# Optimization experiments

Measured on AMD Instinct MI355X. Metric: run time of the kernel, lower is better.

## Reference

```python
import jax, jax.numpy as jnp
import numpy as np
import math

N, K, M = 4, 2048, 1024   # batch, seq_len, dim_in
DQ, DV = 1024, 1024       # dim_q, dim_v


def _xavier_uniform(k, shape, fan_in, fan_out):
    bound = math.sqrt(6.0 / (fan_in + fan_out))
    return jax.random.uniform(k, shape, jnp.float32, -bound, bound)


def setup_inputs() -> dict:
    key = jax.random.key(0)
    ks = jax.random.split(key, 9)
    query = jax.random.normal(ks[0], (N, K, M), jnp.float32)
    key_t = jax.random.normal(ks[1], (N, K, M), jnp.float32)
    value = jax.random.normal(ks[2], (N, K, M), jnp.float32)
    # causal mask: True above diagonal -> masked out (typical production usage)
    mask = jnp.broadcast_to(jnp.triu(jnp.ones((K, K), bool), k=1), (N, K, K))
    Wq = _xavier_uniform(ks[3], (DQ, M), M, DQ)
    bq = jax.random.uniform(ks[4], (DQ,), jnp.float32, -1 / math.sqrt(M), 1 / math.sqrt(M))
    Wk = _xavier_uniform(ks[5], (DQ, M), M, DQ)
    bk = jax.random.uniform(ks[6], (DQ,), jnp.float32, -1 / math.sqrt(M), 1 / math.sqrt(M))
    Wv = _xavier_uniform(ks[7], (DV, M), M, DV)
    bv = jax.random.uniform(ks[8], (DV,), jnp.float32, -1 / math.sqrt(M), 1 / math.sqrt(M))
    return {"query": query, "key": key_t, "value": value, "mask": mask,
            "Wq": Wq, "bq": bq, "Wk": Wk, "bk": bk, "Wv": Wv, "bv": bv}


def reference(query, key, value, mask, Wq, bq, Wk, bk, Wv, bv):
    # linear projections (torch Linear: x @ W.T + b)
    Q = jnp.einsum("nkm,dm->nkd", query, Wq) + bq   # (N, K, DQ)
    Kp = jnp.einsum("nkm,dm->nkd", key, Wk) + bk    # (N, K, DQ)
    V = jnp.einsum("nkm,dm->nkd", value, Wv) + bv   # (N, K, DV)
    # scaled dot product; scale uses projected dim (dim_q)
    scores = jnp.einsum("nqd,nkd->nqk", Q, Kp) / jnp.sqrt(jnp.float32(DQ))
    scores = jnp.where(mask, jnp.float32(-1e9), scores)
    w = jax.nn.softmax(scores, axis=2)               # (N, K, K)
    y = jnp.einsum("nqk,nkd->nqd", w, V)             # (N, K, DV)
    return y
```

## Files before the change

### kernel.cpp

```cpp
#include <hip/hip_runtime.h>
#include <hip/hip_bf16.h>


typedef __bf16 bf16x8 __attribute__((ext_vector_type(8)));
typedef float  f32x4  __attribute__((ext_vector_type(4)));

#define BM 128
#define BN 128
#define BKK 64

__device__ __forceinline__ int swz(int row, int slot) {
    return row * 128 + (((slot) ^ (row & 7)) << 4);
}

__device__ __forceinline__ void gload16(const __bf16* g, __bf16* l) {
    __builtin_amdgcn_global_load_lds((const __attribute__((address_space(1))) void*)g,
                                     (__attribute__((address_space(3))) void*)l, 16, 0, 0);
}

__device__ __forceinline__ void xcd_remap(int& bx, int& by, int& bz) {
    const int nx = gridDim.x, ny = gridDim.y;
    const int nwg = nx * ny * gridDim.z;
    const int flat = blockIdx.x + nx * (blockIdx.y + ny * blockIdx.z);
    const int q = nwg >> 3, r = nwg & 7;
    const int xcd = flat & 7, idx = flat >> 3;
    const int l = (xcd < r ? xcd * (q + 1) : r * (q + 1) + (xcd - r) * q) + idx;
    bx = l % nx; by = (l / nx) % ny; bz = l / (nx * ny);
}

template<int MH, int NH, bool DOA, bool DOB>
__device__ __forceinline__ void phase256(const char* LAb, const char* LBb,
    int wM, int wn, int g, int li,
    bf16x8 (&aF)[4][2], bf16x8 (&bF)[2][2], f32x4 (&acc)[8][4])
{
    if (DOA) {
#pragma unroll
        for (int i = 0; i < 4; i++)
#pragma unroll
            for (int kk = 0; kk < 2; kk++) {
                const int row = wM * 128 + MH * 64 + i * 16 + li;
                aF[i][kk] = *(const bf16x8*)(LAb + swz(row, kk * 4 + g));
            }
    }
    if (DOB) {
#pragma unroll
        for (int j = 0; j < 2; j++)
#pragma unroll
            for (int kk = 0; kk < 2; kk++) {
                const int row = wn * 64 + NH * 32 + j * 16 + li;
                bF[j][kk] = *(const bf16x8*)(LBb + swz(row, kk * 4 + g));
            }
    }
    __builtin_amdgcn_s_barrier();
    __builtin_amdgcn_sched_barrier(0);
    __builtin_amdgcn_s_setprio(1);
#pragma unroll
    for (int kk = 0; kk < 2; kk++)
#pragma unroll
        for (int i = 0; i < 4; i++)
#pragma unroll
            for (int j = 0; j < 2; j++)
                acc[MH * 4 + i][NH * 2 + j] = __builtin_amdgcn_mfma_f32_16x16x32_bf16(
                    aF[i][kk], bF[j][kk], acc[MH * 4 + i][NH * 2 + j], 0, 0, 0);
    __builtin_amdgcn_s_setprio(0);
    __builtin_amdgcn_s_barrier();
    __builtin_amdgcn_sched_barrier(0);
}

__global__ __launch_bounds__(512)
void gemm256_proj(const __bf16* __restrict__ Ap, const __bf16* __restrict__ Bp,
                  const float* __restrict__ b0, const float* __restrict__ b1,
                  const float* __restrict__ b2, float scaleQ, __bf16* __restrict__ Cp)
{
    __shared__ __bf16 LA[2][256 * 64];
    __shared__ __bf16 LB[2][256 * 64];

    int bx, by, bz;
    xcd_remap(bx, by, bz);
    const int m0 = by * 256, n0 = bx * 256;
    const long z = bz;

    const int tid = threadIdx.x;
    const int wid = tid >> 6, lane = tid & 63;
    const int wM = wid >> 2;
    const int wn = wid & 3;
    const int g = lane >> 4, li = lane & 15;
    const int rl = lane >> 3;
    const int sg = (lane & 7) ^ rl;

    const __bf16* Az = Ap + z * 8388608L;
    const __bf16* Bz = Bp + z * 1048576L;

    auto ISSUE = [&](int buf, int k0) {
#pragma unroll
        for (int i = 0; i < 4; i++) {
            const int seg = wid * 4 + i;
            const int r = seg * 8 + rl;
            gload16(Az + (long)(m0 + r) * 1024 + k0 + sg * 8, &LA[buf][seg * 512]);
        }
#pragma unroll
        for (int i = 0; i < 4; i++) {
            const int seg = wid * 4 + i;
            const int r = seg * 8 + rl;
            gload16(Bz + (long)(n0 + r) * 1024 + k0 + sg * 8, &LB[buf][seg * 512]);
        }
    };

    f32x4 acc[8][4];
#pragma unroll
    for (int i = 0; i < 8; i++)
#pragma unroll
        for (int j = 0; j < 4; j++)
            acc[i][j] = (f32x4){0.f, 0.f, 0.f, 0.f};
    bf16x8 aF[4][2], bF[2][2];

    const int nt = 16;
    ISSUE(0, 0);
    int cur = 0;
    for (int t = 0; t < nt; ++t) {
        if (t + 1 < nt) {
            ISSUE(cur ^ 1, (t + 1) * 64);
            __builtin_amdgcn_sched_barrier(0);
            asm volatile("s_waitcnt vmcnt(8)" ::: "memory");
        } else {
            __builtin_amdgcn_sched_barrier(0);
            asm volatile("s_waitcnt vmcnt(0)" ::: "memory");
        }
        __builtin_amdgcn_sched_barrier(0);
        __builtin_amdgcn_s_barrier();
        __builtin_amdgcn_sched_barrier(0);

        const char* LAb = (const char*)&LA[cur][0];
        const char* LBb = (const char*)&LB[cur][0];
        phase256<0, 0, true,  true >(LAb, LBb, wM, wn, g, li, aF, bF, acc);
        phase256<0, 1, false, true >(LAb, LBb, wM, wn, g, li, aF, bF, acc);
        phase256<1, 1, true,  false>(LAb, LBb, wM, wn, g, li, aF, bF, acc);
        phase256<1, 0, false, true >(LAb, LBb, wM, wn, g, li, aF, bF, acc);
        cur ^= 1;
    }

    const float scale = (z == 0) ? scaleQ : 1.f;
    const float* bias = z == 0 ? b0 : (z == 1 ? b1 : b2);
    __bf16* C = Cp + z * 8388608L;
#pragma unroll
    for (int fi = 0; fi < 8; fi++) {
#pragma unroll
        for (int fj = 0; fj < 4; fj++) {
            const int row = m0 + wM * 128 + fi * 16 + g * 4;
            const int col = n0 + wn * 64 + fj * 16 + li;
            const float b = bias[col];
#pragma unroll
            for (int jj = 0; jj < 4; jj++)
                C[(long)(row + jj) * 1024 + col] = (__bf16)((acc[fi][fj][jj] + b) * scale);
        }
    }
}

template<int MODE>
__global__ __launch_bounds__(256)
void gemm_bt(const __bf16* __restrict__ Ap, const __bf16* __restrict__ Bp,
             void* __restrict__ Cp, int Kd, int lda, int ldb, int ldc,
             long strideA, long strideB, long strideC)
{
    __shared__ __bf16 smA[2][BM * BKK];
    __shared__ __bf16 smB[2][BN * BKK];

    int bx, by, bz;
    xcd_remap(bx, by, bz);

    const int tid = threadIdx.x;
    const int m0 = by * BM;
    const int n0 = bx * BN;
    if (MODE == 1 && n0 > m0) return;

    const long z = bz;
    int kEnd = Kd;
    if (MODE == 2) { int lim = m0 + BM; kEnd = lim < Kd ? lim : Kd; }

    const int wid = tid >> 6, lane = tid & 63;
    const int wm = (wid >> 1) * 64, wn = (wid & 1) * 64;
    const int g = lane >> 4, li = lane & 15;
    const int rl = lane >> 3;
    const int sg = (lane & 7) ^ rl;
    const __bf16* Az = Ap + z * strideA;
    const __bf16* Bz = Bp + z * strideB;

    f32x4 acc[4][4];
    for (int i = 0; i < 4; i++)
        for (int j = 0; j < 4; j++)
            acc[i][j] = (f32x4){0.f, 0.f, 0.f, 0.f};

    auto STAGE = [&](int buf, int k0) {
        for (int i = 0; i < 4; i++) {
            const int seg = i * 4 + wid;
            const int r = seg * 8 + rl;
            gload16(Az + (long)(m0 + r) * lda + k0 + sg * 8, &smA[buf][seg * 512]);
            gload16(Bz + (long)(n0 + r) * ldb + k0 + sg * 8, &smB[buf][seg * 512]);
        }
    };

    auto COMPUTE = [&](int buf) {
        for (int kk = 0; kk < 2; kk++) {
            const int slot = kk * 4 + g;
            bf16x8 af[4], bfv[4];
            for (int t = 0; t < 4; t++)
                af[t] = *(const bf16x8*)((const char*)&smA[buf][0] + swz(wm + t * 16 + li, slot));
            for (int t = 0; t < 4; t++)
                bfv[t] = *(const bf16x8*)((const char*)&smB[buf][0] + swz(wn + t * 16 + li, slot));
            for (int tm = 0; tm < 4; tm++)
                for (int tn = 0; tn < 4; tn++)
                    acc[tm][tn] = __builtin_amdgcn_mfma_f32_16x16x32_bf16(
                        af[tm], bfv[tn], acc[tm][tn], 0, 0, 0);
        }
    };

    const int nt = kEnd / BKK;
    STAGE(0, 0);
    __syncthreads();
    int cur = 0;
    for (int t = 0; t < nt - 1; ++t) {
        STAGE(cur ^ 1, (t + 1) * BKK);
        COMPUTE(cur);
        __syncthreads();
        cur ^= 1;
    }
    COMPUTE(cur);

    for (int tm = 0; tm < 4; tm++) {
        for (int tn = 0; tn < 4; tn++) {
            const int row = m0 + wm + tm * 16 + g * 4;
            const int col = n0 + wn + tn * 16 + li;
            float* C = (float*)Cp + z * strideC;
            for (int j = 0; j < 4; j++)
                C[(long)(row + j) * ldc + col] = acc[tm][tn][j];
        }
    }
}

__global__ __launch_bounds__(256)
void cvt3(const float* __restrict__ s0, const float* __restrict__ s1,
          const float* __restrict__ s2, __bf16* __restrict__ d0,
          __bf16* __restrict__ d1, __bf16* __restrict__ d2, long n)
{
    const int zz = blockIdx.y;
    const float* src = zz == 0 ? s0 : (zz == 1 ? s1 : s2);
    __bf16* dst = zz == 0 ? d0 : (zz == 1 ? d1 : d2);
    long i = ((long)blockIdx.x * 256 + threadIdx.x) * 8;
    const long stride = (long)gridDim.x * 2048;
    for (; i < n; i += stride) {
        float4 a = *(const float4*)(src + i);
        float4 b = *(const float4*)(src + i + 4);
        bf16x8 v;
        v[0] = (__bf16)a.x; v[1] = (__bf16)a.y; v[2] = (__bf16)a.z; v[3] = (__bf16)a.w;
        v[4] = (__bf16)b.x; v[5] = (__bf16)b.y; v[6] = (__bf16)b.z; v[7] = (__bf16)b.w;
        *(bf16x8*)(dst + i) = v;
    }
}

__global__ __launch_bounds__(256)
void transpose2d(const ushort* __restrict__ V, ushort* __restrict__ Vt)
{
    __shared__ ushort t[64][65];
    const int d0 = blockIdx.x * 64, k0 = blockIdx.y * 64;
    const long nb = blockIdx.z;
    const ushort* Vb = V + nb * 2048 * 1024;
    ushort* Vtb = Vt + nb * 1024 * 2048;

    for (int i = 0; i < 16; i++) {
        int lin = threadIdx.x + 256 * i;
        int r = lin >> 6, c = lin & 63;
        t[r][c] = Vb[(long)(k0 + r) * 1024 + d0 + c];
    }
    __syncthreads();
    for (int i = 0; i < 16; i++) {
        int lin = threadIdx.x + 256 * i;
        int r = lin >> 6, c = lin & 63;
        Vtb[(long)(d0 + r) * 2048 + k0 + c] = t[c][r];
    }
}

__global__ __launch_bounds__(256)
void softmax_causal(float* __restrict__ S)
{
    const int q = blockIdx.x;
    const long rowoff = (long)blockIdx.y * 2048 + q;
    const float* Srow = S + rowoff * 2048;
    __bf16* Prow = (__bf16*)S + rowoff * 4096;

    const int tid = threadIdx.x;
    const int wid = tid >> 6, lane = tid & 63;

    float v[8];
    float mx = -1e30f;
    for (int i = 0; i < 8; i++) {
        int idx = tid + 256 * i;
        v[i] = (idx <= q) ? Srow[idx] : -1e30f;
        mx = fmaxf(mx, v[i]);
    }
    for (int off = 32; off; off >>= 1) mx = fmaxf(mx, __shfl_xor(mx, off));
    __shared__ float red[8];
    if (lane == 0) red[wid] = mx;
    __syncthreads();
    mx = fmaxf(fmaxf(red[0], red[1]), fmaxf(red[2], red[3]));

    float e[8];
    float s = 0.f;
    for (int i = 0; i < 8; i++) {
        int idx = tid + 256 * i;
        e[i] = (idx <= q) ? __expf(v[i] - mx) : 0.f;
        s += e[i];
    }
    for (int off = 32; off; off >>= 1) s += __shfl_xor(s, off);
    if (lane == 0) red[4 + wid] = s;
    __syncthreads();
    s = red[4] + red[5] + red[6] + red[7];
    const float inv = 1.f / s;

    for (int i = 0; i < 8; i++)
        Prow[tid + 256 * i] = (__bf16)(e[i] * inv);
}

extern "C" void kernel_launch(void* const* d_in, const int* in_sizes, int n_in,
                              void* d_out, int out_size, void* d_ws, size_t ws_size,
                              hipStream_t stream) {
    const float* query = (const float*)d_in[0];
    const float* key   = (const float*)d_in[1];
    const float* value = (const float*)d_in[2];
    const float* Wq = (const float*)d_in[4];
    const float* bq = (const float*)d_in[5];
    const float* Wk = (const float*)d_in[6];
    const float* bk = (const float*)d_in[7];
    const float* Wv = (const float*)d_in[8];
    const float* bv = (const float*)d_in[9];
    float* out = (float*)d_out;

    char* ws = (char*)d_ws;
    const long MB = 1L << 20;
    __bf16* QKV = (__bf16*)(ws);
    __bf16* Vp  = QKV + 2 * 8388608L;
    __bf16* Vt  = (__bf16*)(ws + 48 * MB);
    float*  S   = (float*) (ws + 64 * MB);
    __bf16* Xb  = (__bf16*)(ws + 64 * MB);
    __bf16* Wb  = (__bf16*)(ws + 112 * MB);

    const dim3 blk(256);
    const long nX = 2048L * 1024 * 4;
    const long nW = 1024L * 1024;

    cvt3<<<dim3(1024, 3), blk, 0, stream>>>(query, key, value,
        Xb, Xb + 8388608L, Xb + 2 * 8388608L, nX);
    cvt3<<<dim3(512, 3), blk, 0, stream>>>(Wq, Wk, Wv,
        Wb, Wb + 1048576L, Wb + 2 * 1048576L, nW);

    gemm256_proj<<<dim3(4, 32, 3), dim3(512), 0, stream>>>(
        Xb, Wb, bq, bk, bv, 1.f / 32.f, QKV);

    transpose2d<<<dim3(16, 32, 4), blk, 0, stream>>>((const ushort*)Vp, (ushort*)Vt);

    gemm_bt<1><<<dim3(16, 16, 4), blk, 0, stream>>>(QKV, QKV + 8388608L, S,
        1024, 1024, 1024, 2048, 2048L * 1024, 2048L * 1024, 2048L * 2048);

    softmax_causal<<<dim3(2048, 4), blk, 0, stream>>>(S);

    gemm_bt<2><<<dim3(8, 16, 4), blk, 0, stream>>>((__bf16*)S, Vt, out,
        2048, 4096, 2048, 1024, 2048L * 4096, 1024L * 2048, 2048L * 1024);
}
```

Baseline: 212.4 us.

## Restructure projection GEMM into quadrant-interleaved pipeline with split global loads

Rewrites the 256x256 projection GEMM main loop so each wave computes four 32x64 sub-tiles, one in each 128x128 quadrant, instead of one 128x64 block. The next tile's global-to-LDS loads are split into four quarters and issued between the MFMA phases, with vmcnt waits placed so loads overlap compute more finely. This is meant to hide global-load latency and balance LDS reads against MFMA work. It adds barriers per phase and holds more B fragments in registers, which may raise register pressure. A redundant prefetch is issued on the last iteration.

```diff
diff --git a/kernel.cpp b/kernel.cpp
--- a/kernel.cpp
+++ b/kernel.cpp
@@ -28,44 +28,10 @@
     bx = l % nx; by = (l / nx) % ny; bz = l / (nx * ny);
 }
 
-template<int MH, int NH, bool DOA, bool DOB>
-__device__ __forceinline__ void phase256(const char* LAb, const char* LBb,
-    int wM, int wn, int g, int li,
-    bf16x8 (&aF)[4][2], bf16x8 (&bF)[2][2], f32x4 (&acc)[8][4])
-{
-    if (DOA) {
-#pragma unroll
-        for (int i = 0; i < 4; i++)
-#pragma unroll
-            for (int kk = 0; kk < 2; kk++) {
-                const int row = wM * 128 + MH * 64 + i * 16 + li;
-                aF[i][kk] = *(const bf16x8*)(LAb + swz(row, kk * 4 + g));
-            }
-    }
-    if (DOB) {
-#pragma unroll
-        for (int j = 0; j < 2; j++)
-#pragma unroll
-            for (int kk = 0; kk < 2; kk++) {
-                const int row = wn * 64 + NH * 32 + j * 16 + li;
-                bF[j][kk] = *(const bf16x8*)(LBb + swz(row, kk * 4 + g));
-            }
-    }
-    __builtin_amdgcn_s_barrier();
-    __builtin_amdgcn_sched_barrier(0);
-    __builtin_amdgcn_s_setprio(1);
-#pragma unroll
-    for (int kk = 0; kk < 2; kk++)
-#pragma unroll
-        for (int i = 0; i < 4; i++)
-#pragma unroll
-            for (int j = 0; j < 2; j++)
-                acc[MH * 4 + i][NH * 2 + j] = __builtin_amdgcn_mfma_f32_16x16x32_bf16(
-                    aF[i][kk], bF[j][kk], acc[MH * 4 + i][NH * 2 + j], 0, 0, 0);
-    __builtin_amdgcn_s_setprio(0);
-    __builtin_amdgcn_s_barrier();
-    __builtin_amdgcn_sched_barrier(0);
-}
+#define SBAR()  do { __builtin_amdgcn_s_barrier(); __builtin_amdgcn_sched_barrier(0); } while (0)
+#define VMCNT4() do { __builtin_amdgcn_sched_barrier(0); \
+                      asm volatile("s_waitcnt vmcnt(4)" ::: "memory"); \
+                      __builtin_amdgcn_sched_barrier(0); } while (0)
 
 __global__ __launch_bounds__(512)
 void gemm256_proj(const __bf16* __restrict__ Ap, const __bf16* __restrict__ Bp,
@@ -82,8 +48,8 @@
 
     const int tid = threadIdx.x;
     const int wid = tid >> 6, lane = tid & 63;
-    const int wM = wid >> 2;
-    const int wn = wid & 3;
+    const int wr = wid >> 1;
+    const int wc = wid & 1;
     const int g = lane >> 4, li = lane & 15;
     const int rl = lane >> 3;
     const int sg = (lane & 7) ^ rl;
@@ -91,69 +57,116 @@
     const __bf16* Az = Ap + z * 8388608L;
     const __bf16* Bz = Bp + z * 1048576L;
 
-    auto ISSUE = [&](int buf, int k0) {
-#pragma unroll
-        for (int i = 0; i < 4; i++) {
-            const int seg = wid * 4 + i;
-            const int r = seg * 8 + rl;
-            gload16(Az + (long)(m0 + r) * 1024 + k0 + sg * 8, &LA[buf][seg * 512]);
+    auto ISSUE_HALF = [&](int buf, int k0, int h) {
+        const bool isA = (h == 0 || h == 3);
+        const int rowoff = (h == 0 || h == 1) ? 0 : 128;
+        const __bf16* src = isA ? Az : Bz;
+        const int base0 = isA ? m0 : n0;
+        __bf16* dst = (isA ? &LA[buf][0] : &LB[buf][0]) + rowoff * 64;
+#pragma unroll
+        for (int i = 0; i < 2; i++) {
+            const int seg = wid * 2 + i;
+            const int r = rowoff + seg * 8 + rl;
+            gload16(src + (long)(base0 + r) * 1024 + k0 + sg * 8, dst + seg * 512);
         }
-#pragma unroll
-        for (int i = 0; i < 4; i++) {
-            const int seg = wid * 4 + i;
-            const int r = seg * 8 + rl;
-            gload16(Bz + (long)(n0 + r) * 1024 + k0 + sg * 8, &LB[buf][seg * 512]);
-        }
-    };
-
-    f32x4 acc[8][4];
-#pragma unroll
-    for (int i = 0; i < 8; i++)
-#pragma unroll
-        for (int j = 0; j < 4; j++)
-            acc[i][j] = (f32x4){0.f, 0.f, 0.f, 0.f};
-    bf16x8 aF[4][2], bF[2][2];
+    };
+
+    bf16x8 aF[2][2];
+    bf16x8 bF[2][4][2];
+    f32x4 acc[4][2][4];
+#pragma unroll
+    for (int q2 = 0; q2 < 4; q2++)
+#pragma unroll
+        for (int fi = 0; fi < 2; fi++)
+#pragma unroll
+            for (int fj = 0; fj < 4; fj++)
+                acc[q2][fi][fj] = (f32x4){0.f, 0.f, 0.f, 0.f};
+
+    auto DSREAD_A = [&](int buf, int qm) {
+#pragma unroll
+        for (int fi = 0; fi < 2; fi++)
+#pragma unroll
+            for (int kk = 0; kk < 2; kk++)
+                aF[fi][kk] = *(const bf16x8*)((const char*)&LA[buf][0] +
+                    swz(qm * 128 + wr * 32 + fi * 16 + li, kk * 4 + g));
+    };
+    auto DSREAD_B = [&](int buf, int qn) {
+#pragma unroll
+        for (int fj = 0; fj < 4; fj++)
+#pragma unroll
+            for (int kk = 0; kk < 2; kk++)
+                bF[qn][fj][kk] = *(const bf16x8*)((const char*)&LB[buf][0] +
+                    swz(qn * 128 + wc * 64 + fj * 16 + li, kk * 4 + g));
+    };
+    auto MFMA16 = [&](int qm, int qn) {
+        __builtin_amdgcn_s_setprio(1);
+#pragma unroll
+        for (int kk = 0; kk < 2; kk++)
+#pragma unroll
+            for (int fi = 0; fi < 2; fi++)
+#pragma unroll
+                for (int fj = 0; fj < 4; fj++)
+                    acc[qm * 2 + qn][fi][fj] = __builtin_amdgcn_mfma_f32_16x16x32_bf16(
+                        aF[fi][kk], bF[qn][fj][kk], acc[qm * 2 + qn][fi][fj], 0, 0, 0);
+        __builtin_amdgcn_s_setprio(0);
+    };
 
     const int nt = 16;
-    ISSUE(0, 0);
+    ISSUE_HALF(0, 0, 0); ISSUE_HALF(0, 0, 1); ISSUE_HALF(0, 0, 2); ISSUE_HALF(0, 0, 3);
+    VMCNT4();
+    SBAR();
+
     int cur = 0;
     for (int t = 0; t < nt; ++t) {
-        if (t + 1 < nt) {
-            ISSUE(cur ^ 1, (t + 1) * 64);
-            __builtin_amdgcn_sched_barrier(0);
-            asm volatile("s_waitcnt vmcnt(8)" ::: "memory");
-        } else {
-            __builtin_amdgcn_sched_barrier(0);
-            asm volatile("s_waitcnt vmcnt(0)" ::: "memory");
-        }
-        __builtin_amdgcn_sched_barrier(0);
-        __builtin_amdgcn_s_barrier();
-        __builtin_amdgcn_sched_barrier(0);
-
-        const char* LAb = (const char*)&LA[cur][0];
-        const char* LBb = (const char*)&LB[cur][0];
-        phase256<0, 0, true,  true >(LAb, LBb, wM, wn, g, li, aF, bF, acc);
-        phase256<0, 1, false, true >(LAb, LBb, wM, wn, g, li, aF, bF, acc);
-        phase256<1, 1, true,  false>(LAb, LBb, wM, wn, g, li, aF, bF, acc);
-        phase256<1, 0, false, true >(LAb, LBb, wM, wn, g, li, aF, bF, acc);
-        cur ^= 1;
-    }
+        const int nxt = cur ^ 1;
+        const int k0n = (t + 1 < nt) ? (t + 1) * 64 : 0;
+
+        DSREAD_A(cur, 0); DSREAD_B(cur, 0);
+        ISSUE_HALF(nxt, k0n, 0);
+        VMCNT4();
+        SBAR();
+        MFMA16(0, 0);
+        SBAR();
+        DSREAD_B(cur, 1);
+        ISSUE_HALF(nxt, k0n, 1);
+        VMCNT4();
+        SBAR();
+        MFMA16(0, 1);
+        SBAR();
+        DSREAD_A(cur, 1);
+        ISSUE_HALF(nxt, k0n, 2);
+        SBAR();
+        MFMA16(1, 1);
+        SBAR();
+        ISSUE_HALF(nxt, k0n, 3);
+        VMCNT4();
+        SBAR();
+        MFMA16(1, 0);
+        SBAR();
+        cur = nxt;
+    }
+    __builtin_amdgcn_sched_barrier(0);
+    asm volatile("s_waitcnt vmcnt(0)" ::: "memory");
 
     const float scale = (z == 0) ? scaleQ : 1.f;
     const float* bias = z == 0 ? b0 : (z == 1 ? b1 : b2);
     __bf16* C = Cp + z * 8388608L;
 #pragma unroll
-    for (int fi = 0; fi < 8; fi++) {
-#pragma unroll
-        for (int fj = 0; fj < 4; fj++) {
-            const int row = m0 + wM * 128 + fi * 16 + g * 4;
-            const int col = n0 + wn * 64 + fj * 16 + li;
-            const float b = bias[col];
-#pragma unroll
-            for (int jj = 0; jj < 4; jj++)
-                C[(long)(row + jj) * 1024 + col] = (__bf16)((acc[fi][fj][jj] + b) * scale);
-        }
-    }
+    for (int qm = 0; qm < 2; qm++)
+#pragma unroll
+        for (int qn = 0; qn < 2; qn++)
+#pragma unroll
+            for (int fi = 0; fi < 2; fi++)
+#pragma unroll
+                for (int fj = 0; fj < 4; fj++) {
+                    const int row = m0 + qm * 128 + wr * 32 + fi * 16 + g * 4;
+                    const int col = n0 + qn * 128 + wc * 64 + fj * 16 + li;
+                    const float b = bias[col];
+#pragma unroll
+                    for (int jj = 0; jj < 4; jj++)
+                        C[(long)(row + jj) * 1024 + col] =
+                            (__bf16)((acc[qm * 2 + qn][fi][fj][jj] + b) * scale);
+                }
 }
 
 template<int MODE>
```

Result: faster. 206.9 us (-2.6%).
